# Performance work log

Hardware: AMD Instinct MI355X
Metric: run time of the kernel (lower is better)

## Reference

```python
import jax, jax.numpy as jnp
import numpy as np


def setup_inputs() -> dict:
    key = jax.random.key(0)
    k1, k2 = jax.random.split(key)
    B, EMB, CODES, NUM_TOKENS = 16, 64, 16384, 1024
    x_in = jax.random.normal(k1, (B, EMB, CODES), dtype=jnp.float32)
    code_embedding = jax.random.uniform(k2, (NUM_TOKENS, EMB), dtype=jnp.float32)
    return {"x_in": x_in, "code_embedding": code_embedding}


def reference(x_in, code_embedding):
    # x_in: [B, emb, codes]; code_embedding: [num_tokens, emb]
    x_t = jnp.transpose(x_in, (0, 2, 1))  # [B, codes, emb]
    # squared euclidean distances (argmin is invariant to sqrt used by cdist)
    x2 = jnp.sum(x_t * x_t, axis=-1)                      # [B, codes]
    e2 = jnp.sum(code_embedding * code_embedding, axis=-1)  # [num_tokens]
    dots = jnp.einsum('bce,ke->bck', x_t, code_embedding)   # [B, codes, num_tokens]
    dist2 = x2[:, :, None] - 2.0 * dots + e2[None, None, :]
    indices = jnp.argmin(dist2, axis=2)                   # [B, codes]
    x_out = jnp.transpose(code_embedding[indices], (0, 2, 1))  # [B, emb, codes]
    return x_out, indices[:, :, None]  # indices keepdim like torch argmin(keepdim=True)
```

## Files before the change

kernel.cpp:

```cpp
#include <hip/hip_runtime.h>


#define BB 16
#define EMB 64
#define CODES 16384
#define NT 1024
#define NTILES 64

typedef __attribute__((ext_vector_type(8))) short s16x8;
typedef __attribute__((ext_vector_type(4))) float f32x4;
typedef __attribute__((ext_vector_type(4))) int i32x4;
typedef unsigned int u32;

__device__ inline short bf16_hi(float f) { return (short)(__builtin_bit_cast(u32, f) >> 16); }
__device__ inline float hi_part(float f) { return __builtin_bit_cast(float, __builtin_bit_cast(u32, f) & 0xFFFF0000u); }
__device__ inline u32 umin_(u32 a, u32 b) { return a < b ? a : b; }
__device__ inline u32 umax_(u32 a, u32 b) { return a > b ? a : b; }

__global__ __launch_bounds__(256) void vq_prep(const float* __restrict__ E,
                                               char* __restrict__ wsE,
                                               float* __restrict__ wsh) {
  const int bid = blockIdx.x, tid = threadIdx.x;
  if (bid < 32) {
    const int gid = bid * 256 + tid;
    const int nt = gid >> 7, ks = (gid >> 6) & 1, lane = gid & 63;
    const int col = lane & 15, quad = lane >> 4;
    const int n = nt * 16 + col;
    const int k0 = ks * 32 + quad * 8;
    const float* ep = E + n * EMB + k0;
    s16x8 hv, lv;
    #pragma unroll
    for (int j = 0; j < 8; ++j) {
      float v = ep[j];
      float hf = hi_part(v);
      hv[j] = bf16_hi(v);
      lv[j] = bf16_hi(v - hf);
    }
    char* base = wsE + ((size_t)nt << 12) + ((size_t)ks << 10) + lane * 16;
    *(i32x4*)(base)        = __builtin_bit_cast(i32x4, hv);
    *(i32x4*)(base + 2048) = __builtin_bit_cast(i32x4, lv);
  } else {
    const int n = (bid - 32) * 256 + tid;
    if (n < NT) {
      const float4* ep = (const float4*)(E + n * EMB);
      float s = 0.f;
      #pragma unroll
      for (int g = 0; g < 16; ++g) { float4 v = ep[g]; s += v.x*v.x + v.y*v.y + v.z*v.z + v.w*v.w; }
      wsh[n] = -0.5f * s;
    }
  }
}

__global__ __launch_bounds__(256, 3) void vq_main(
    const float* __restrict__ x, const float* __restrict__ E,
    const char* __restrict__ wsE, const float* __restrict__ wsh,
    float* __restrict__ xout, float* __restrict__ iout) {
  __shared__ uint2 cand[256];
  const int tid = threadIdx.x;
  const int wave = tid >> 6, lane = tid & 63;
  const int col = lane & 15, quad = lane >> 4;
  const int b = blockIdx.y;
  const int c0 = blockIdx.x * 256;
  const int cw = c0 + wave * 64;

  s16x8 ah[4][2], al[4][2];
  #pragma unroll
  for (int mt = 0; mt < 4; ++mt) {
    #pragma unroll
    for (int ks = 0; ks < 2; ++ks) {
      s16x8 hv, lv;
      #pragma unroll
      for (int j = 0; j < 8; ++j) {
        const int e = ks * 32 + quad * 8 + j;
        float v = x[((size_t)b * EMB + e) * CODES + (size_t)(cw + mt * 16 + col)];
        float hf = hi_part(v);
        hv[j] = bf16_hi(v);
        lv[j] = bf16_hi(v - hf);
      }
      ah[mt][ks] = hv;
      al[mt][ks] = lv;
    }
  }

  u32 k1[4][4], k2[4][4];
  #pragma unroll
  for (int mt = 0; mt < 4; ++mt)
    #pragma unroll
    for (int r = 0; r < 4; ++r) { k1[mt][r] = 0u; k2[mt][r] = 0u; }

  u32 inv = 1023u - (u32)col;
  const char* p = wsE + lane * 16;
  const float* hp = wsh + col;

  for (int nt = 0; nt < NTILES; ++nt) {
    s16x8 bh0 = __builtin_bit_cast(s16x8, *(const i32x4*)(p));
    s16x8 bh1 = __builtin_bit_cast(s16x8, *(const i32x4*)(p + 1024));
    s16x8 bl0 = __builtin_bit_cast(s16x8, *(const i32x4*)(p + 2048));
    s16x8 bl1 = __builtin_bit_cast(s16x8, *(const i32x4*)(p + 3072));
    const float hl = *hp;
    const float C = fmaf(hl, 16384.f, 96.f * 16384.f);

    f32x4 acc[4];
    #pragma unroll
    for (int mt = 0; mt < 4; ++mt) {
      acc[mt] = (f32x4){0.f, 0.f, 0.f, 0.f};
      acc[mt] = __builtin_amdgcn_mfma_f32_16x16x32_bf16(ah[mt][0], bh0, acc[mt], 0, 0, 0);
      acc[mt] = __builtin_amdgcn_mfma_f32_16x16x32_bf16(ah[mt][1], bh1, acc[mt], 0, 0, 0);
      acc[mt] = __builtin_amdgcn_mfma_f32_16x16x32_bf16(al[mt][0], bh0, acc[mt], 0, 0, 0);
      acc[mt] = __builtin_amdgcn_mfma_f32_16x16x32_bf16(al[mt][1], bh1, acc[mt], 0, 0, 0);
      acc[mt] = __builtin_amdgcn_mfma_f32_16x16x32_bf16(ah[mt][0], bl0, acc[mt], 0, 0, 0);
      acc[mt] = __builtin_amdgcn_mfma_f32_16x16x32_bf16(ah[mt][1], bl1, acc[mt], 0, 0, 0);
    }

    #pragma unroll
    for (int mt = 0; mt < 4; ++mt) {
      #pragma unroll
      for (int r = 0; r < 4; ++r) {
        u32 q = (u32)fmaf(acc[mt][r], 16384.f, C);
        u32 key = (q << 10) + inv;
        u32 t = umin_(key, k1[mt][r]);
        k1[mt][r] = umax_(key, k1[mt][r]);
        k2[mt][r] = umax_(t, k2[mt][r]);
      }
    }
    inv -= 16u;
    p += 4096;
    hp += 16;
  }

  #pragma unroll
  for (int mt = 0; mt < 4; ++mt) {
    #pragma unroll
    for (int r = 0; r < 4; ++r) {
      u32 a1 = k1[mt][r], a2 = k2[mt][r];
      #pragma unroll
      for (int m = 1; m <= 8; m <<= 1) {
        u32 r1 = __shfl_xor(a1, m, 64);
        u32 r2 = __shfl_xor(a2, m, 64);
        u32 t = umin_(a1, r1);
        a1 = umax_(a1, r1);
        a2 = umax_(umax_(a2, r2), t);
      }
      if (col == r) cand[wave * 64 + mt * 16 + quad * 4 + r] = make_uint2(a1, a2);
    }
  }
  __syncthreads();

  const u32 K1 = cand[tid].x, K2 = cand[tid].y;
  const int i1 = 1023 - (int)(K1 & 1023u);
  const int i2 = 1023 - (int)(K2 & 1023u);
  const float* xq = x + (size_t)b * EMB * CODES + (size_t)(c0 + tid);
  const float4* e1 = (const float4*)(E + i1 * EMB);
  const float4* e2 = (const float4*)(E + i2 * EMB);
  float d10 = 0, d11 = 0, d12 = 0, d13 = 0, d20 = 0, d21 = 0, d22 = 0, d23 = 0;
  #pragma unroll
  for (int g = 0; g < 16; ++g) {
    float4 a = e1[g], c4 = e2[g];
    float x0 = xq[(size_t)(4 * g + 0) * CODES];
    float x1 = xq[(size_t)(4 * g + 1) * CODES];
    float x2 = xq[(size_t)(4 * g + 2) * CODES];
    float x3 = xq[(size_t)(4 * g + 3) * CODES];
    d10 = fmaf(x0, a.x, d10);  d11 = fmaf(x1, a.y, d11);
    d12 = fmaf(x2, a.z, d12);  d13 = fmaf(x3, a.w, d13);
    d20 = fmaf(x0, c4.x, d20); d21 = fmaf(x1, c4.y, d21);
    d22 = fmaf(x2, c4.z, d22); d23 = fmaf(x3, c4.w, d23);
  }
  const float s1 = ((d10 + d11) + (d12 + d13)) + wsh[i1];
  const float s2 = ((d20 + d21) + (d22 + d23)) + wsh[i2];
  const bool take2 = (s2 > s1) || (s2 == s1 && i2 < i1);
  const int idx = take2 ? i2 : i1;

  const float* Er = E + idx * EMB;
  float* xo = xout + (size_t)b * EMB * CODES + (size_t)(c0 + tid);
  #pragma unroll
  for (int e = 0; e < EMB; ++e) xo[(size_t)e * CODES] = Er[e];
  iout[(size_t)b * CODES + (size_t)(c0 + tid)] = (float)idx;
}

extern "C" void kernel_launch(void* const* d_in, const int* in_sizes, int n_in,
                              void* d_out, int out_size, void* d_ws, size_t ws_size,
                              hipStream_t stream) {
  const float* x = (const float*)d_in[0];
  const float* E = (const float*)d_in[1];
  float* xout = (float*)d_out;
  float* iout = (float*)d_out + (size_t)BB * EMB * CODES;

  char* wsE = (char*)d_ws;
  float* wsh = (float*)((char*)d_ws + (256 << 10));

  vq_prep<<<36, 256, 0, stream>>>(E, wsE, wsh);
  vq_main<<<dim3(CODES / 256, BB), 256, 0, stream>>>(x, E, wsE, wsh, xout, iout);
}
```

Measured before the change: 243.1 us.

## Prefetch codebook tiles, fold bias into MFMA accumulator, use single-wave blocks

Software-pipelines the per-tile codebook fragment loads one iteration ahead and unrolls the tile loop. Pre-scales x by 16384 and initializes the accumulator with a precomputed scaled norm bias, which removes the per-element fma before key packing. Blocks shrink to one wave (64 threads) with more blocks in flight. The prefetch reads one tile past the end into workspace padding and raises register pressure.

```diff
diff --git a/kernel.cpp b/kernel.cpp
--- a/kernel.cpp
+++ b/kernel.cpp
@@ -17,9 +17,14 @@
 __device__ inline u32 umin_(u32 a, u32 b) { return a < b ? a : b; }
 __device__ inline u32 umax_(u32 a, u32 b) { return a > b ? a : b; }
 
+#define WSE_OFF   0
+#define WSH_OFF   266240
+#define WSH2_OFF  270336
+
 __global__ __launch_bounds__(256) void vq_prep(const float* __restrict__ E,
                                                char* __restrict__ wsE,
-                                               float* __restrict__ wsh) {
+                                               float* __restrict__ wsh,
+                                               float* __restrict__ wsh2) {
   const int bid = blockIdx.x, tid = threadIdx.x;
   if (bid < 32) {
     const int gid = bid * 256 + tid;
@@ -46,22 +51,23 @@
       float s = 0.f;
       #pragma unroll
       for (int g = 0; g < 16; ++g) { float4 v = ep[g]; s += v.x*v.x + v.y*v.y + v.z*v.z + v.w*v.w; }
-      wsh[n] = -0.5f * s;
+      const float h = -0.5f * s;
+      wsh[n] = h;
+      wsh2[n] = 16384.f * (h + 128.f);
     }
   }
 }
 
-__global__ __launch_bounds__(256, 3) void vq_main(
+__global__ __launch_bounds__(64, 2) void vq_main(
     const float* __restrict__ x, const float* __restrict__ E,
     const char* __restrict__ wsE, const float* __restrict__ wsh,
+    const float* __restrict__ wsh2,
     float* __restrict__ xout, float* __restrict__ iout) {
-  __shared__ uint2 cand[256];
-  const int tid = threadIdx.x;
-  const int wave = tid >> 6, lane = tid & 63;
+  __shared__ uint2 cand[64];
+  const int lane = threadIdx.x;
   const int col = lane & 15, quad = lane >> 4;
   const int b = blockIdx.y;
-  const int c0 = blockIdx.x * 256;
-  const int cw = c0 + wave * 64;
+  const int c0 = blockIdx.x * 64;
 
   s16x8 ah[4][2], al[4][2];
   #pragma unroll
@@ -72,7 +78,7 @@
       #pragma unroll
       for (int j = 0; j < 8; ++j) {
         const int e = ks * 32 + quad * 8 + j;
-        float v = x[((size_t)b * EMB + e) * CODES + (size_t)(cw + mt * 16 + col)];
+        float v = x[((size_t)b * EMB + e) * CODES + (size_t)(c0 + mt * 16 + col)] * 16384.f;
         float hf = hi_part(v);
         hv[j] = bf16_hi(v);
         lv[j] = bf16_hi(v - hf);
@@ -90,20 +96,33 @@
 
   u32 inv = 1023u - (u32)col;
   const char* p = wsE + lane * 16;
-  const float* hp = wsh + col;
-
+  const float* hp = wsh2 + col;
+
+  i32x4 nb0 = *(const i32x4*)(p);
+  i32x4 nb1 = *(const i32x4*)(p + 1024);
+  i32x4 nb2 = *(const i32x4*)(p + 2048);
+  i32x4 nb3 = *(const i32x4*)(p + 3072);
+  float nch = *hp;
+
+  #pragma unroll 4
   for (int nt = 0; nt < NTILES; ++nt) {
-    s16x8 bh0 = __builtin_bit_cast(s16x8, *(const i32x4*)(p));
-    s16x8 bh1 = __builtin_bit_cast(s16x8, *(const i32x4*)(p + 1024));
-    s16x8 bl0 = __builtin_bit_cast(s16x8, *(const i32x4*)(p + 2048));
-    s16x8 bl1 = __builtin_bit_cast(s16x8, *(const i32x4*)(p + 3072));
-    const float hl = *hp;
-    const float C = fmaf(hl, 16384.f, 96.f * 16384.f);
+    const s16x8 bh0 = __builtin_bit_cast(s16x8, nb0);
+    const s16x8 bh1 = __builtin_bit_cast(s16x8, nb1);
+    const s16x8 bl0 = __builtin_bit_cast(s16x8, nb2);
+    const s16x8 bl1 = __builtin_bit_cast(s16x8, nb3);
+    const float ch = nch;
+
+    p += 4096; hp += 16;
+    nb0 = *(const i32x4*)(p);
+    nb1 = *(const i32x4*)(p + 1024);
+    nb2 = *(const i32x4*)(p + 2048);
+    nb3 = *(const i32x4*)(p + 3072);
+    nch = *hp;
 
     f32x4 acc[4];
     #pragma unroll
     for (int mt = 0; mt < 4; ++mt) {
-      acc[mt] = (f32x4){0.f, 0.f, 0.f, 0.f};
+      acc[mt] = (f32x4){ch, ch, ch, ch};
       acc[mt] = __builtin_amdgcn_mfma_f32_16x16x32_bf16(ah[mt][0], bh0, acc[mt], 0, 0, 0);
       acc[mt] = __builtin_amdgcn_mfma_f32_16x16x32_bf16(ah[mt][1], bh1, acc[mt], 0, 0, 0);
       acc[mt] = __builtin_amdgcn_mfma_f32_16x16x32_bf16(al[mt][0], bh0, acc[mt], 0, 0, 0);
@@ -116,7 +135,7 @@
     for (int mt = 0; mt < 4; ++mt) {
       #pragma unroll
       for (int r = 0; r < 4; ++r) {
-        u32 q = (u32)fmaf(acc[mt][r], 16384.f, C);
+        u32 q = (u32)acc[mt][r];
         u32 key = (q << 10) + inv;
         u32 t = umin_(key, k1[mt][r]);
         k1[mt][r] = umax_(key, k1[mt][r]);
@@ -124,8 +143,6 @@
       }
     }
     inv -= 16u;
-    p += 4096;
-    hp += 16;
   }
 
   #pragma unroll
@@ -141,15 +158,15 @@
         a1 = umax_(a1, r1);
         a2 = umax_(umax_(a2, r2), t);
       }
-      if (col == r) cand[wave * 64 + mt * 16 + quad * 4 + r] = make_uint2(a1, a2);
+      if (col == r) cand[mt * 16 + quad * 4 + r] = make_uint2(a1, a2);
     }
   }
   __syncthreads();
 
-  const u32 K1 = cand[tid].x, K2 = cand[tid].y;
+  const u32 K1 = cand[lane].x, K2 = cand[lane].y;
   const int i1 = 1023 - (int)(K1 & 1023u);
   const int i2 = 1023 - (int)(K2 & 1023u);
-  const float* xq = x + (size_t)b * EMB * CODES + (size_t)(c0 + tid);
+  const float* xq = x + (size_t)b * EMB * CODES + (size_t)(c0 + lane);
   const float4* e1 = (const float4*)(E + i1 * EMB);
   const float4* e2 = (const float4*)(E + i2 * EMB);
   float d10 = 0, d11 = 0, d12 = 0, d13 = 0, d20 = 0, d21 = 0, d22 = 0, d23 = 0;
@@ -171,10 +188,10 @@
   const int idx = take2 ? i2 : i1;
 
   const float* Er = E + idx * EMB;
-  float* xo = xout + (size_t)b * EMB * CODES + (size_t)(c0 + tid);
+  float* xo = xout + (size_t)b * EMB * CODES + (size_t)(c0 + lane);
   #pragma unroll
   for (int e = 0; e < EMB; ++e) xo[(size_t)e * CODES] = Er[e];
-  iout[(size_t)b * CODES + (size_t)(c0 + tid)] = (float)idx;
+  iout[(size_t)b * CODES + (size_t)(c0 + lane)] = (float)idx;
 }
 
 extern "C" void kernel_launch(void* const* d_in, const int* in_sizes, int n_in,
@@ -185,9 +202,10 @@
   float* xout = (float*)d_out;
   float* iout = (float*)d_out + (size_t)BB * EMB * CODES;
 
-  char* wsE = (char*)d_ws;
-  float* wsh = (float*)((char*)d_ws + (256 << 10));
-
-  vq_prep<<<36, 256, 0, stream>>>(E, wsE, wsh);
-  vq_main<<<dim3(CODES / 256, BB), 256, 0, stream>>>(x, E, wsE, wsh, xout, iout);
+  char* wsE  = (char*)d_ws + WSE_OFF;
+  float* wsh  = (float*)((char*)d_ws + WSH_OFF);
+  float* wsh2 = (float*)((char*)d_ws + WSH2_OFF);
+
+  vq_prep<<<36, 256, 0, stream>>>(E, wsE, wsh, wsh2);
+  vq_main<<<dim3(CODES / 64, BB), 64, 0, stream>>>(x, E, wsE, wsh, wsh2, xout, iout);
 }
```

Result: faster. 225.8 us (-7.1%).

## Stage codebook tiles in LDS with async double-buffered loads, fold bias into MFMA

Applied to the files above, without the earlier changes.

The main loop no longer reads the bf16 split codebook straight from global memory on every tile. Tiles are staged into LDS in chunks of four through global_load_lds async copies, with double buffering so the next chunk loads while the current one is computed. The scaled bias is precomputed in the prep kernel and used as the initial MFMA accumulator, and x is pre-scaled by 16384, which removes the per-element fma before conversion. The cost is 36KB of LDS per block, which may limit occupancy, plus a __syncthreads per chunk.

```diff
diff --git a/kernel.cpp b/kernel.cpp
--- a/kernel.cpp
+++ b/kernel.cpp
@@ -6,6 +6,8 @@
 #define CODES 16384
 #define NT 1024
 #define NTILES 64
+#define CHUNK 4
+#define EPOCHS (NTILES / CHUNK)
 
 typedef __attribute__((ext_vector_type(8))) short s16x8;
 typedef __attribute__((ext_vector_type(4))) float f32x4;
@@ -17,9 +19,21 @@
 __device__ inline u32 umin_(u32 a, u32 b) { return a < b ? a : b; }
 __device__ inline u32 umax_(u32 a, u32 b) { return a > b ? a : b; }
 
+__device__ inline void async_copy16(const char* g, char* lds_base_uniform) {
+  __builtin_amdgcn_global_load_lds(
+      (const __attribute__((address_space(1))) unsigned int*)g,
+      (__attribute__((address_space(3))) unsigned int*)(unsigned int)(unsigned long long)lds_base_uniform,
+      16, 0, 0);
+}
+
+#define WSE_OFF   0
+#define WSH_OFF   266240
+#define WSH2_OFF  270336
+
 __global__ __launch_bounds__(256) void vq_prep(const float* __restrict__ E,
                                                char* __restrict__ wsE,
-                                               float* __restrict__ wsh) {
+                                               float* __restrict__ wsh,
+                                               float* __restrict__ wsh2) {
   const int bid = blockIdx.x, tid = threadIdx.x;
   if (bid < 32) {
     const int gid = bid * 256 + tid;
@@ -46,7 +60,9 @@
       float s = 0.f;
       #pragma unroll
       for (int g = 0; g < 16; ++g) { float4 v = ep[g]; s += v.x*v.x + v.y*v.y + v.z*v.z + v.w*v.w; }
-      wsh[n] = -0.5f * s;
+      const float h = -0.5f * s;
+      wsh[n] = h;
+      wsh2[n] = 16384.f * (h + 128.f);
     }
   }
 }
@@ -54,8 +70,10 @@
 __global__ __launch_bounds__(256, 3) void vq_main(
     const float* __restrict__ x, const float* __restrict__ E,
     const char* __restrict__ wsE, const float* __restrict__ wsh,
+    const float* __restrict__ wsh2,
     float* __restrict__ xout, float* __restrict__ iout) {
-  __shared__ uint2 cand[256];
+  __shared__ char smem[2 * CHUNK * 4096 + 4096];
+  float* lh = (float*)(smem + 2 * CHUNK * 4096);
   const int tid = threadIdx.x;
   const int wave = tid >> 6, lane = tid & 63;
   const int col = lane & 15, quad = lane >> 4;
@@ -63,6 +81,16 @@
   const int c0 = blockIdx.x * 256;
   const int cw = c0 + wave * 64;
 
+  ((float4*)lh)[tid] = ((const float4*)wsh2)[tid];
+  {
+    const char* g = wsE + wave * 4096 + lane * 16;
+    char* lb = smem + wave * 4096;
+    async_copy16(g,        lb);
+    async_copy16(g + 1024, lb + 1024);
+    async_copy16(g + 2048, lb + 2048);
+    async_copy16(g + 3072, lb + 3072);
+  }
+
   s16x8 ah[4][2], al[4][2];
   #pragma unroll
   for (int mt = 0; mt < 4; ++mt) {
@@ -72,7 +100,7 @@
       #pragma unroll
       for (int j = 0; j < 8; ++j) {
         const int e = ks * 32 + quad * 8 + j;
-        float v = x[((size_t)b * EMB + e) * CODES + (size_t)(cw + mt * 16 + col)];
+        float v = x[((size_t)b * EMB + e) * CODES + (size_t)(cw + mt * 16 + col)] * 16384.f;
         float hf = hi_part(v);
         hv[j] = bf16_hi(v);
         lv[j] = bf16_hi(v - hf);
@@ -89,45 +117,58 @@
     for (int r = 0; r < 4; ++r) { k1[mt][r] = 0u; k2[mt][r] = 0u; }
 
   u32 inv = 1023u - (u32)col;
-  const char* p = wsE + lane * 16;
-  const float* hp = wsh + col;
-
-  for (int nt = 0; nt < NTILES; ++nt) {
-    s16x8 bh0 = __builtin_bit_cast(s16x8, *(const i32x4*)(p));
-    s16x8 bh1 = __builtin_bit_cast(s16x8, *(const i32x4*)(p + 1024));
-    s16x8 bl0 = __builtin_bit_cast(s16x8, *(const i32x4*)(p + 2048));
-    s16x8 bl1 = __builtin_bit_cast(s16x8, *(const i32x4*)(p + 3072));
-    const float hl = *hp;
-    const float C = fmaf(hl, 16384.f, 96.f * 16384.f);
-
-    f32x4 acc[4];
-    #pragma unroll
-    for (int mt = 0; mt < 4; ++mt) {
-      acc[mt] = (f32x4){0.f, 0.f, 0.f, 0.f};
-      acc[mt] = __builtin_amdgcn_mfma_f32_16x16x32_bf16(ah[mt][0], bh0, acc[mt], 0, 0, 0);
-      acc[mt] = __builtin_amdgcn_mfma_f32_16x16x32_bf16(ah[mt][1], bh1, acc[mt], 0, 0, 0);
-      acc[mt] = __builtin_amdgcn_mfma_f32_16x16x32_bf16(al[mt][0], bh0, acc[mt], 0, 0, 0);
-      acc[mt] = __builtin_amdgcn_mfma_f32_16x16x32_bf16(al[mt][1], bh1, acc[mt], 0, 0, 0);
-      acc[mt] = __builtin_amdgcn_mfma_f32_16x16x32_bf16(ah[mt][0], bl0, acc[mt], 0, 0, 0);
-      acc[mt] = __builtin_amdgcn_mfma_f32_16x16x32_bf16(ah[mt][1], bl1, acc[mt], 0, 0, 0);
-    }
-
-    #pragma unroll
-    for (int mt = 0; mt < 4; ++mt) {
-      #pragma unroll
-      for (int r = 0; r < 4; ++r) {
-        u32 q = (u32)fmaf(acc[mt][r], 16384.f, C);
-        u32 key = (q << 10) + inv;
-        u32 t = umin_(key, k1[mt][r]);
-        k1[mt][r] = umax_(key, k1[mt][r]);
-        k2[mt][r] = umax_(t, k2[mt][r]);
-      }
-    }
-    inv -= 16u;
-    p += 4096;
-    hp += 16;
-  }
-
+
+  __syncthreads();
+
+  for (int c = 0; c < EPOCHS; ++c) {
+    if (c < EPOCHS - 1) {
+      const char* g = wsE + (size_t)(c + 1) * (CHUNK * 4096) + wave * 4096 + lane * 16;
+      char* lb = smem + ((c + 1) & 1) * (CHUNK * 4096) + wave * 4096;
+      async_copy16(g,        lb);
+      async_copy16(g + 1024, lb + 1024);
+      async_copy16(g + 2048, lb + 2048);
+      async_copy16(g + 3072, lb + 3072);
+    }
+
+    const char* rb = smem + (c & 1) * (CHUNK * 4096) + lane * 16;
+    #pragma unroll
+    for (int t = 0; t < CHUNK; ++t) {
+      const char* p = rb + t * 4096;
+      const s16x8 bh0 = __builtin_bit_cast(s16x8, *(const i32x4*)(p));
+      const s16x8 bh1 = __builtin_bit_cast(s16x8, *(const i32x4*)(p + 1024));
+      const s16x8 bl0 = __builtin_bit_cast(s16x8, *(const i32x4*)(p + 2048));
+      const s16x8 bl1 = __builtin_bit_cast(s16x8, *(const i32x4*)(p + 3072));
+      const float ch = lh[(c * CHUNK + t) * 16 + col];
+      const f32x4 cq = (f32x4){ch, ch, ch, ch};
+
+      f32x4 acc[4];
+      #pragma unroll
+      for (int mt = 0; mt < 4; ++mt) {
+        acc[mt] = __builtin_amdgcn_mfma_f32_16x16x32_bf16(ah[mt][0], bh0, cq, 0, 0, 0);
+        acc[mt] = __builtin_amdgcn_mfma_f32_16x16x32_bf16(ah[mt][1], bh1, acc[mt], 0, 0, 0);
+        acc[mt] = __builtin_amdgcn_mfma_f32_16x16x32_bf16(al[mt][0], bh0, acc[mt], 0, 0, 0);
+        acc[mt] = __builtin_amdgcn_mfma_f32_16x16x32_bf16(al[mt][1], bh1, acc[mt], 0, 0, 0);
+        acc[mt] = __builtin_amdgcn_mfma_f32_16x16x32_bf16(ah[mt][0], bl0, acc[mt], 0, 0, 0);
+        acc[mt] = __builtin_amdgcn_mfma_f32_16x16x32_bf16(ah[mt][1], bl1, acc[mt], 0, 0, 0);
+      }
+
+      #pragma unroll
+      for (int mt = 0; mt < 4; ++mt) {
+        #pragma unroll
+        for (int r = 0; r < 4; ++r) {
+          u32 q = (u32)acc[mt][r];
+          u32 key = (q << 10) + inv;
+          u32 tt = umin_(key, k1[mt][r]);
+          k1[mt][r] = umax_(key, k1[mt][r]);
+          k2[mt][r] = umax_(tt, k2[mt][r]);
+        }
+      }
+      inv -= 16u;
+    }
+    __syncthreads();
+  }
+
+  uint2* cand = (uint2*)smem;
   #pragma unroll
   for (int mt = 0; mt < 4; ++mt) {
     #pragma unroll
@@ -170,11 +211,11 @@
   const bool take2 = (s2 > s1) || (s2 == s1 && i2 < i1);
   const int idx = take2 ? i2 : i1;
 
+  iout[(size_t)b * CODES + (size_t)(c0 + tid)] = (float)idx;
   const float* Er = E + idx * EMB;
   float* xo = xout + (size_t)b * EMB * CODES + (size_t)(c0 + tid);
   #pragma unroll
   for (int e = 0; e < EMB; ++e) xo[(size_t)e * CODES] = Er[e];
-  iout[(size_t)b * CODES + (size_t)(c0 + tid)] = (float)idx;
 }
 
 extern "C" void kernel_launch(void* const* d_in, const int* in_sizes, int n_in,
@@ -185,9 +226,10 @@
   float* xout = (float*)d_out;
   float* iout = (float*)d_out + (size_t)BB * EMB * CODES;
 
-  char* wsE = (char*)d_ws;
-  float* wsh = (float*)((char*)d_ws + (256 << 10));
-
-  vq_prep<<<36, 256, 0, stream>>>(E, wsE, wsh);
-  vq_main<<<dim3(CODES / 256, BB), 256, 0, stream>>>(x, E, wsE, wsh, xout, iout);
-}
+  char* wsE  = (char*)d_ws + WSE_OFF;
+  float* wsh  = (float*)((char*)d_ws + WSH_OFF);
+  float* wsh2 = (float*)((char*)d_ws + WSH2_OFF);
+
+  vq_prep<<<36, 256, 0, stream>>>(E, wsE, wsh, wsh2);
+  vq_main<<<dim3(CODES / 256, BB), 256, 0, stream>>>(x, E, wsE, wsh, wsh2, xout, iout);
+}
```

Measured after the change: 203.1 us. -16.5%, faster.
